# Kernel optimization log

Measured on AMD Instinct MI355X. Metric: run time of the kernel, lower is better.

## Reference

```python
import jax, jax.numpy as jnp
import numpy as np
import math

D_MODEL = 768
B, S = 8, 2048


def setup_inputs() -> dict:
    key = jax.random.key(0)
    k1, k2, k3, k4, k5 = jax.random.split(key, 5)
    return {
        "input": jax.random.normal(k1, (B, S, D_MODEL), dtype=jnp.float32),
        "attention_mask": jax.random.randint(k2, (B,), 0, S + 1, dtype=jnp.int32),
        "Wq": jax.random.normal(k3, (D_MODEL, D_MODEL), dtype=jnp.float32),
        "Wk": jax.random.normal(k4, (D_MODEL, D_MODEL), dtype=jnp.float32),
        "Wv": jax.random.normal(k5, (D_MODEL, D_MODEL), dtype=jnp.float32),
    }


def reference(input, attention_mask, Wq, Wk, Wv):
    d_model = Wq.shape[0]
    # QKV projections (v is computed in the original but never used in the output)
    q = jnp.matmul(input, Wq)  # [B,S,D]
    k = jnp.matmul(input, Wk)  # [B,S,D]
    v = jnp.matmul(input, Wv)  # [B,S,D] (dead in original forward output)
    # Per-sample QK^T, vectorized instead of the original python loop+cat
    attention_score = jnp.einsum("bqd,bkd->bqk", q, k) / math.sqrt(float(d_model) ** 3)
    # Ragged mask: positions (j,k) with j<len_i and k<len_i keep the score, else -1000.
    # Built with vectorized arange comparisons instead of the original triple python loop.
    idx = jnp.arange(attention_score.shape[1])  # [S]
    valid = idx[None, :] < attention_mask[:, None]  # [B,S]
    keep = valid[:, :, None] & valid[:, None, :]  # [B,S,S]
    mask_attention_score = jnp.where(keep, attention_score, jnp.float32(-1000.0))
    attention_score_n = jax.nn.softmax(mask_attention_score, axis=-1)  # computed but unused, as in original
    # Original returns UNMASKED, pre-softmax scores matmul'd with the raw input (not v).
    self_attention = jnp.einsum("bqk,bkd->bqd", attention_score, input)
    return self_attention
```

## Files before the change

### kernel.cpp

```cpp
#include <hip/hip_runtime.h>
#include <cmath>


typedef __attribute__((ext_vector_type(8))) short short8;
typedef __attribute__((ext_vector_type(4))) float f32x4;

__device__ __forceinline__ unsigned short f2bf(float f) {
    union { float f; unsigned int u; } v; v.f = f;
    unsigned int u = v.u;
    return (unsigned short)((u + 0x7FFFu + ((u >> 16) & 1u)) >> 16);
}

template <int NIT>
__device__ __forceinline__ void setup_stage(const unsigned short* base, int ld, int tid,
                                            const unsigned short* (&gp)[NIT])
{
    #pragma unroll
    for (int it = 0; it < NIT; ++it) {
        int slot = it * 256 + tid, r = slot >> 3, c = slot & 7;
        gp[it] = base + (size_t)r * ld + ((c ^ (r & 7)) << 3);
    }
}

template <int NIT>
__device__ __forceinline__ void stage_adv(const unsigned short* const (&gp)[NIT], int koff,
                                          unsigned short* ldsbase, int tid)
{
    #pragma unroll
    for (int it = 0; it < NIT; ++it) {
        unsigned short* lp = ldsbase + (size_t)(it * 256 + (tid & 192)) * 8;
        __builtin_amdgcn_global_load_lds(
            (__attribute__((address_space(1))) void*)(void*)(gp[it] + koff),
            (__attribute__((address_space(3))) void*)lp, 16, 0, 0);
    }
}

template <int F>
__device__ __forceinline__ void frag_offs(int wbase, int l15, int quad, int (&o)[F][2])
{
    #pragma unroll
    for (int i = 0; i < F; ++i) {
        int r = wbase + i * 16 + l15;
        o[i][0] = r * 64 + ((quad ^ (r & 7)) << 3);
        o[i][1] = r * 64 + (((quad + 4) ^ (r & 7)) << 3);
    }
}

template <int FM, int FN>
__device__ __forceinline__ void mfma_frags(const unsigned short* __restrict__ Al,
                                           const unsigned short* __restrict__ Bl,
                                           const int (&oA)[FM][2], const int (&oB)[FN][2],
                                           f32x4 (&acc)[FM][FN])
{
    short8 af[FM][2], bfr[FN][2];
    #pragma unroll
    for (int i = 0; i < FM; ++i) {
        af[i][0] = *reinterpret_cast<const short8*>(&Al[oA[i][0]]);
        af[i][1] = *reinterpret_cast<const short8*>(&Al[oA[i][1]]);
    }
    #pragma unroll
    for (int i = 0; i < FN; ++i) {
        bfr[i][0] = *reinterpret_cast<const short8*>(&Bl[oB[i][0]]);
        bfr[i][1] = *reinterpret_cast<const short8*>(&Bl[oB[i][1]]);
    }
    #pragma unroll
    for (int ks = 0; ks < 2; ++ks)
        #pragma unroll
        for (int mi = 0; mi < FM; ++mi)
            #pragma unroll
            for (int ni = 0; ni < FN; ++ni)
                acc[mi][ni] = __builtin_amdgcn_mfma_f32_16x16x32_bf16(
                    af[mi][ks], bfr[ni][ks], acc[mi][ni], 0, 0, 0);
}

template <int ROWS>
__device__ __forceinline__ void stage_f32(const float* __restrict__ src, unsigned short* lds,
                                          int ld, int tid)
{
    #pragma unroll
    for (int it = 0; it < ROWS / 32; ++it) {
        int slot = it * 256 + tid;
        int r = slot >> 3, c = slot & 7;
        const float* gp = src + (size_t)r * ld + c * 8;
        float4 a = *reinterpret_cast<const float4*>(gp);
        float4 d = *reinterpret_cast<const float4*>(gp + 4);
        union { short8 s; unsigned short u[8]; } v;
        v.u[0] = f2bf(a.x); v.u[1] = f2bf(a.y); v.u[2] = f2bf(a.z); v.u[3] = f2bf(a.w);
        v.u[4] = f2bf(d.x); v.u[5] = f2bf(d.y); v.u[6] = f2bf(d.z); v.u[7] = f2bf(d.w);
        *reinterpret_cast<short8*>(&lds[r * 64 + ((c ^ (r & 7)) << 3)]) = v.s;
    }
}

__device__ __forceinline__ void store_c(float* C, size_t i, float v) { C[i] = v; }
__device__ __forceinline__ void store_c(unsigned short* C, size_t i, float v) { C[i] = f2bf(v); }

template <int TM, int TN, typename CT>
__device__ __forceinline__ void epilogue(CT* __restrict__ C, f32x4 (&acc)[TM / 32][TN / 32],
                                         int rowBase, int colBase, int ldc, float alpha,
                                         int wr, int wc, int l15, int quad)
{
    #pragma unroll
    for (int mi = 0; mi < TM / 32; ++mi)
        #pragma unroll
        for (int ni = 0; ni < TN / 32; ++ni) {
            int col = colBase + wc + ni * 16 + l15;
            #pragma unroll
            for (int r = 0; r < 4; ++r) {
                int row = rowBase + wr + mi * 16 + quad * 4 + r;
                store_c(C, (size_t)row * ldc + col, alpha * acc[mi][ni][r]);
            }
        }
}

__global__ __launch_bounds__(256)
void prep(const float* __restrict__ X, unsigned short* __restrict__ Xt,
          unsigned short* __restrict__ Xbf)
{
    __shared__ unsigned short T[64 * 64];
    const int blk = blockIdx.x;
    const int b = blk & 7;
    const int tile = blk >> 3;
    const int s0 = (tile & 31) * 64;
    const int d0 = (tile >> 5) * 64;
    const float* Xb = X + (size_t)b * 2048 * 768;
    unsigned short* Xtb = Xt + (size_t)b * 2048 * 768;
    unsigned short* Xbb = Xbf + (size_t)b * 2048 * 768;

    const int mr = threadIdx.x >> 4;
    const int mc = threadIdx.x & 15;

    const float* src = &Xb[(size_t)(s0 + 4 * mr) * 768 + d0 + 4 * mc];
    float4 v0 = *reinterpret_cast<const float4*>(src);
    float4 v1 = *reinterpret_cast<const float4*>(src + 768);
    float4 v2 = *reinterpret_cast<const float4*>(src + 2 * 768);
    float4 v3 = *reinterpret_cast<const float4*>(src + 3 * 768);
    ushort4 r0 = { f2bf(v0.x), f2bf(v0.y), f2bf(v0.z), f2bf(v0.w) };
    ushort4 r1 = { f2bf(v1.x), f2bf(v1.y), f2bf(v1.z), f2bf(v1.w) };
    ushort4 r2 = { f2bf(v2.x), f2bf(v2.y), f2bf(v2.z), f2bf(v2.w) };
    ushort4 r3 = { f2bf(v3.x), f2bf(v3.y), f2bf(v3.z), f2bf(v3.w) };
    unsigned short* dstb = &Xbb[(size_t)(s0 + 4 * mr) * 768 + d0 + 4 * mc];
    *reinterpret_cast<ushort4*>(dstb)            = r0;
    *reinterpret_cast<ushort4*>(dstb + 768)      = r1;
    *reinterpret_cast<ushort4*>(dstb + 2 * 768)  = r2;
    *reinterpret_cast<ushort4*>(dstb + 3 * 768)  = r3;

    ushort4 c0 = { r0.x, r1.x, r2.x, r3.x };
    ushort4 c1 = { r0.y, r1.y, r2.y, r3.y };
    ushort4 c2 = { r0.z, r1.z, r2.z, r3.z };
    ushort4 c3 = { r0.w, r1.w, r2.w, r3.w };
    {
        int d;
        d = 4 * mc + 0; *reinterpret_cast<ushort4*>(&T[d * 64 + ((mr ^ (2 * (d & 7))) & 15) * 4]) = c0;
        d = 4 * mc + 1; *reinterpret_cast<ushort4*>(&T[d * 64 + ((mr ^ (2 * (d & 7))) & 15) * 4]) = c1;
        d = 4 * mc + 2; *reinterpret_cast<ushort4*>(&T[d * 64 + ((mr ^ (2 * (d & 7))) & 15) * 4]) = c2;
        d = 4 * mc + 3; *reinterpret_cast<ushort4*>(&T[d * 64 + ((mr ^ (2 * (d & 7))) & 15) * 4]) = c3;
    }
    __syncthreads();
    #pragma unroll
    for (int p = 0; p < 2; ++p) {
        int d  = p * 32 + (threadIdx.x >> 3);
        int q0 = 2 * (threadIdx.x & 7);
        int c  = (q0 ^ (2 * (d & 7))) & 15;
        short8 o = *reinterpret_cast<const short8*>(&T[d * 64 + c * 4]);
        *reinterpret_cast<short8*>(&Xtb[(size_t)(d0 + d) * 2048 + s0 + q0 * 4]) = o;
    }
}

__global__ __launch_bounds__(256)
void gemm_GP(const unsigned short* __restrict__ Xt, unsigned short* __restrict__ G16,
             const float* __restrict__ Wq, const float* __restrict__ Wk,
             unsigned short* __restrict__ P16)
{
    __shared__ unsigned short lds[2][(64 + 64) * 64];
    const int blk = blockIdx.x;
    const int tid = threadIdx.x, lane = tid & 63, wave = tid >> 6;
    const int l15 = lane & 15, quad = lane >> 4;
    const int wr = (wave >> 1) * 32, wc = (wave & 1) * 32;

    if (blk < 624) {
        const int b = blk & 7;
        const int u = blk >> 3;
        int ty = 0, rem = u, len = 12;
        while (rem >= len) { rem -= len; --len; ++ty; }
        const int tz = ty + rem;
        const bool diag = (ty == tz);

        const unsigned short* Xtb = Xt + (size_t)b * 768 * 2048;
        const unsigned short* A0 = Xtb + (size_t)ty * 64 * 2048;
        const unsigned short* B0 = Xtb + (size_t)tz * 64 * 2048;
        unsigned short* C = G16 + (size_t)b * 768 * 768;

        const unsigned short* gA[2]; const unsigned short* gB[2];
        setup_stage<2>(A0, 2048, tid, gA);
        setup_stage<2>(B0, 2048, tid, gB);
        int oA[2][2], oB[2][2];
        frag_offs<2>(wr, l15, quad, oA);
        frag_offs<2>(wc, l15, quad, oB);
        const int bbase = diag ? 0 : 64 * 64;

        f32x4 acc[2][2] = {};
        stage_adv<2>(gA, 0, &lds[0][0], tid);
        if (!diag) stage_adv<2>(gB, 0, &lds[0][64 * 64], tid);
        __syncthreads();

        const int nt = 32;
        for (int t = 0; t < nt; ++t) {
            const int cur = t & 1;
            if (t + 1 < nt) {
                stage_adv<2>(gA, (t + 1) * 64, &lds[cur ^ 1][0], tid);
                if (!diag) stage_adv<2>(gB, (t + 1) * 64, &lds[cur ^ 1][64 * 64], tid);
            }
            mfma_frags<2, 2>(&lds[cur][0], &lds[cur][bbase], oA, oB, acc);
            __syncthreads();
        }

        #pragma unroll
        for (int mi = 0; mi < 2; ++mi)
            #pragma unroll
            for (int ni = 0; ni < 2; ++ni) {
                int col = tz * 64 + wc + ni * 16 + l15;
                int row0 = ty * 64 + wr + mi * 16 + quad * 4;
                ushort4 m;
                m.x = f2bf(acc[mi][ni][0]);
                m.y = f2bf(acc[mi][ni][1]);
                m.z = f2bf(acc[mi][ni][2]);
                m.w = f2bf(acc[mi][ni][3]);
                C[(size_t)(row0 + 0) * 768 + col] = m.x;
                C[(size_t)(row0 + 1) * 768 + col] = m.y;
                C[(size_t)(row0 + 2) * 768 + col] = m.z;
                C[(size_t)(row0 + 3) * 768 + col] = m.w;
                if (!diag)
                    *reinterpret_cast<ushort4*>(&C[(size_t)col * 768 + row0]) = m;
            }
    } else {
        const int pb = blk - 624;
        const int ty = pb / 12, tz = pb - ty * 12;
        int oA[2][2], oB[2][2];
        frag_offs<2>(wr, l15, quad, oA);
        frag_offs<2>(wc, l15, quad, oB);
        f32x4 acc[2][2] = {};
        for (int k0 = 0; k0 < 768; k0 += 64) {
            stage_f32<64>(Wq + (size_t)ty * 64 * 768 + k0, &lds[0][0], 768, tid);
            stage_f32<64>(Wk + (size_t)tz * 64 * 768 + k0, &lds[0][64 * 64], 768, tid);
            __syncthreads();
            mfma_frags<2, 2>(&lds[0][0], &lds[0][64 * 64], oA, oB, acc);
            __syncthreads();
        }
        epilogue<64, 64, unsigned short>(P16, acc, ty * 64, tz * 64, 768, 1.0f,
                                         wr, wc, l15, quad);
    }
}

__global__ __launch_bounds__(256)
void gemm_Ht(const unsigned short* __restrict__ G16, const unsigned short* __restrict__ P16,
             unsigned short* __restrict__ Ht, float alpha)
{
    __shared__ unsigned short lds[2][(96 + 96) * 64];
    const int b = blockIdx.x, ty = blockIdx.y, tz = blockIdx.z;
    const int tid = threadIdx.x, lane = tid & 63, wave = tid >> 6;
    const int wr = (wave >> 1) * 48, wc = (wave & 1) * 48;
    const int l15 = lane & 15, quad = lane >> 4;

    const unsigned short* A0 = G16 + (size_t)b * 768 * 768 + (size_t)ty * 96 * 768;
    const unsigned short* B0 = P16 + (size_t)tz * 96 * 768;

    const unsigned short* gA[3]; const unsigned short* gB[3];
    setup_stage<3>(A0, 768, tid, gA);
    setup_stage<3>(B0, 768, tid, gB);
    int oA[3][2], oB[3][2];
    frag_offs<3>(wr, l15, quad, oA);
    frag_offs<3>(wc, l15, quad, oB);

    f32x4 acc[3][3] = {};
    stage_adv<3>(gA, 0, &lds[0][0], tid);
    stage_adv<3>(gB, 0, &lds[0][96 * 64], tid);
    __syncthreads();

    const int nt = 12;
    for (int t = 0; t < nt; ++t) {
        const int cur = t & 1;
        if (t + 1 < nt) {
            stage_adv<3>(gA, (t + 1) * 64, &lds[cur ^ 1][0], tid);
            stage_adv<3>(gB, (t + 1) * 64, &lds[cur ^ 1][96 * 64], tid);
        }
        mfma_frags<3, 3>(&lds[cur][0], &lds[cur][96 * 64], oA, oB, acc);
        __syncthreads();
    }
    epilogue<96, 96, unsigned short>(Ht + (size_t)b * 768 * 768, acc,
                                     ty * 96, tz * 96, 768, alpha, wr, wc, l15, quad);
}

__global__ __launch_bounds__(256)
void gemm_out(const unsigned short* __restrict__ Xbf, const unsigned short* __restrict__ Ht,
              float* __restrict__ out)
{
    __shared__ unsigned short lds[2][(128 + 128) * 64];
    const int b = blockIdx.x, ty = blockIdx.y, tz = blockIdx.z;
    const int tid = threadIdx.x, lane = tid & 63, wave = tid >> 6;
    const int wr = (wave >> 1) * 64, wc = (wave & 1) * 64;
    const int l15 = lane & 15, quad = lane >> 4;

    const unsigned short* A0 = Xbf + (size_t)b * 2048 * 768 + (size_t)ty * 128 * 768;
    const unsigned short* B0 = Ht + (size_t)b * 768 * 768 + (size_t)tz * 128 * 768;

    const unsigned short* gA[4]; const unsigned short* gB[4];
    setup_stage<4>(A0, 768, tid, gA);
    setup_stage<4>(B0, 768, tid, gB);
    int oA[4][2], oB[4][2];
    frag_offs<4>(wr, l15, quad, oA);
    frag_offs<4>(wc, l15, quad, oB);

    f32x4 acc[4][4] = {};
    stage_adv<4>(gA, 0, &lds[0][0], tid);
    stage_adv<4>(gB, 0, &lds[0][128 * 64], tid);
    __syncthreads();

    const int nt = 12;
    for (int t = 0; t < nt; ++t) {
        const int cur = t & 1;
        if (t + 1 < nt) {
            stage_adv<4>(gA, (t + 1) * 64, &lds[cur ^ 1][0], tid);
            stage_adv<4>(gB, (t + 1) * 64, &lds[cur ^ 1][128 * 64], tid);
        }
        mfma_frags<4, 4>(&lds[cur][0], &lds[cur][128 * 64], oA, oB, acc);
        __syncthreads();
    }
    epilogue<128, 128, float>(out + (size_t)b * 2048 * 768, acc,
                              ty * 128, tz * 128, 768, 1.0f, wr, wc, l15, quad);
}

extern "C" void kernel_launch(void* const* d_in, const int* in_sizes, int n_in,
                              void* d_out, int out_size, void* d_ws, size_t ws_size,
                              hipStream_t stream)
{
    const float* X  = (const float*)d_in[0];
    const float* Wq = (const float*)d_in[2];
    const float* Wk = (const float*)d_in[3];
    float* out = (float*)d_out;

    const int Bn = 8, S = 2048, D = 768;
    const float alpha = 1.0f / (768.0f * sqrtf(768.0f));
    const size_t szX  = (size_t)Bn * S * D;
    const size_t szDD = (size_t)Bn * D * D;

    unsigned short* Xt  = (unsigned short*)d_ws;
    unsigned short* Xbf = Xt + szX;
    unsigned short* P16 = Xbf + szX;
    unsigned short* G16 = P16 + (size_t)D * D;
    unsigned short* Ht  = G16 + szDD;

    prep<<<dim3(Bn * (S / 64) * (D / 64)), 256, 0, stream>>>(X, Xt, Xbf);

    gemm_GP<<<dim3(768), 256, 0, stream>>>(Xt, G16, Wq, Wk, P16);

    gemm_Ht<<<dim3(Bn, 8, 8), 256, 0, stream>>>(G16, P16, Ht, alpha);

    gemm_out<<<dim3(Bn, S / 128, 6), 256, 0, stream>>>(Xbf, Ht, out);
}
```

Before: 180.6 us.

## Fuse Ht and output GEMMs into one persistent kernel with per-batch grid barrier

```diff
diff --git a/kernel.cpp b/kernel.cpp
--- a/kernel.cpp
+++ b/kernel.cpp
@@ -9,6 +9,27 @@
     union { float f; unsigned int u; } v; v.f = f;
     unsigned int u = v.u;
     return (unsigned short)((u + 0x7FFFu + ((u >> 16) & 1u)) >> 16);
+}
+
+__device__ unsigned g_tbar[8][64];
+
+__device__ __forceinline__ void abarrier(unsigned* cnt, unsigned* gen, unsigned n)
+{
+    __syncthreads();
+    if (threadIdx.x == 0) {
+        __threadfence();
+        unsigned g = __hip_atomic_load(gen, __ATOMIC_RELAXED, __HIP_MEMORY_SCOPE_AGENT);
+        unsigned c = __hip_atomic_fetch_add(cnt, 1u, __ATOMIC_ACQ_REL, __HIP_MEMORY_SCOPE_AGENT);
+        if (c == n - 1u) {
+            __hip_atomic_store(cnt, 0u, __ATOMIC_RELAXED, __HIP_MEMORY_SCOPE_AGENT);
+            __hip_atomic_store(gen, g + 1u, __ATOMIC_RELEASE, __HIP_MEMORY_SCOPE_AGENT);
+        } else {
+            while (__hip_atomic_load(gen, __ATOMIC_RELAXED, __HIP_MEMORY_SCOPE_AGENT) == g)
+                __builtin_amdgcn_s_sleep(2);
+        }
+        __threadfence();
+    }
+    __syncthreads();
 }
 
 template <int NIT>
@@ -252,81 +273,74 @@
 }
 
 __global__ __launch_bounds__(256)
-void gemm_Ht(const unsigned short* __restrict__ G16, const unsigned short* __restrict__ P16,
-             unsigned short* __restrict__ Ht, float alpha)
-{
-    __shared__ unsigned short lds[2][(96 + 96) * 64];
-    const int b = blockIdx.x, ty = blockIdx.y, tz = blockIdx.z;
+void ht_out(const unsigned short* __restrict__ G16, const unsigned short* __restrict__ P16,
+            unsigned short* __restrict__ Ht, const unsigned short* __restrict__ Xbf,
+            float* __restrict__ out, float alpha)
+{
+    __shared__ unsigned short lds[(128 + 64) * 64];
+    const int blk = blockIdx.x;
+    const int b  = blk & 7;
+    const int lr = blk >> 3;
     const int tid = threadIdx.x, lane = tid & 63, wave = tid >> 6;
-    const int wr = (wave >> 1) * 48, wc = (wave & 1) * 48;
     const int l15 = lane & 15, quad = lane >> 4;
 
-    const unsigned short* A0 = G16 + (size_t)b * 768 * 768 + (size_t)ty * 96 * 768;
-    const unsigned short* B0 = P16 + (size_t)tz * 96 * 768;
-
-    const unsigned short* gA[3]; const unsigned short* gB[3];
-    setup_stage<3>(A0, 768, tid, gA);
-    setup_stage<3>(B0, 768, tid, gB);
-    int oA[3][2], oB[3][2];
-    frag_offs<3>(wr, l15, quad, oA);
-    frag_offs<3>(wc, l15, quad, oB);
-
-    f32x4 acc[3][3] = {};
-    stage_adv<3>(gA, 0, &lds[0][0], tid);
-    stage_adv<3>(gB, 0, &lds[0][96 * 64], tid);
-    __syncthreads();
-
-    const int nt = 12;
-    for (int t = 0; t < nt; ++t) {
-        const int cur = t & 1;
-        if (t + 1 < nt) {
-            stage_adv<3>(gA, (t + 1) * 64, &lds[cur ^ 1][0], tid);
-            stage_adv<3>(gB, (t + 1) * 64, &lds[cur ^ 1][96 * 64], tid);
-        }
-        mfma_frags<3, 3>(&lds[cur][0], &lds[cur][96 * 64], oA, oB, acc);
-        __syncthreads();
-    }
-    epilogue<96, 96, unsigned short>(Ht + (size_t)b * 768 * 768, acc,
-                                     ty * 96, tz * 96, 768, alpha, wr, wc, l15, quad);
-}
-
-__global__ __launch_bounds__(256)
-void gemm_out(const unsigned short* __restrict__ Xbf, const unsigned short* __restrict__ Ht,
-              float* __restrict__ out)
-{
-    __shared__ unsigned short lds[2][(128 + 128) * 64];
-    const int b = blockIdx.x, ty = blockIdx.y, tz = blockIdx.z;
-    const int tid = threadIdx.x, lane = tid & 63, wave = tid >> 6;
-    const int wr = (wave >> 1) * 64, wc = (wave & 1) * 64;
-    const int l15 = lane & 15, quad = lane >> 4;
-
-    const unsigned short* A0 = Xbf + (size_t)b * 2048 * 768 + (size_t)ty * 128 * 768;
-    const unsigned short* B0 = Ht + (size_t)b * 768 * 768 + (size_t)tz * 128 * 768;
-
-    const unsigned short* gA[4]; const unsigned short* gB[4];
-    setup_stage<4>(A0, 768, tid, gA);
-    setup_stage<4>(B0, 768, tid, gB);
-    int oA[4][2], oB[4][2];
-    frag_offs<4>(wr, l15, quad, oA);
-    frag_offs<4>(wc, l15, quad, oB);
-
-    f32x4 acc[4][4] = {};
-    stage_adv<4>(gA, 0, &lds[0][0], tid);
-    stage_adv<4>(gB, 0, &lds[0][128 * 64], tid);
-    __syncthreads();
-
-    const int nt = 12;
-    for (int t = 0; t < nt; ++t) {
-        const int cur = t & 1;
-        if (t + 1 < nt) {
-            stage_adv<4>(gA, (t + 1) * 64, &lds[cur ^ 1][0], tid);
-            stage_adv<4>(gB, (t + 1) * 64, &lds[cur ^ 1][128 * 64], tid);
-        }
-        mfma_frags<4, 4>(&lds[cur][0], &lds[cur][128 * 64], oA, oB, acc);
-        __syncthreads();
-    }
-    epilogue<128, 128, float>(out + (size_t)b * 2048 * 768, acc,
-                              ty * 128, tz * 128, 768, 1.0f, wr, wc, l15, quad);
+    {
+        const int wr = (wave >> 1) * 32, wc = (wave & 1) * 32;
+        int oA[2][2], oB[2][2];
+        frag_offs<2>(wr, l15, quad, oA);
+        frag_offs<2>(wc, l15, quad, oB);
+        const int nrep = (lr < 48) ? 2 : 1;
+        for (int rep = 0; rep < nrep; ++rep) {
+            const int u = lr + rep * 96;
+            const int ty = u / 12, tz = u - (u / 12) * 12;
+            const unsigned short* A0 = G16 + (size_t)b * 768 * 768 + (size_t)ty * 64 * 768;
+            const unsigned short* B0 = P16 + (size_t)tz * 64 * 768;
+            const unsigned short* gA[2]; const unsigned short* gB[2];
+            setup_stage<2>(A0, 768, tid, gA);
+            setup_stage<2>(B0, 768, tid, gB);
+            f32x4 acc[2][2] = {};
+            for (int k0 = 0; k0 < 768; k0 += 64) {
+                stage_adv<2>(gA, k0, lds, tid);
+                stage_adv<2>(gB, k0, lds + 64 * 64, tid);
+                __syncthreads();
+                mfma_frags<2, 2>(lds, lds + 64 * 64, oA, oB, acc);
+                __syncthreads();
+            }
+            epilogue<64, 64, unsigned short>(Ht + (size_t)b * 768 * 768, acc,
+                                             ty * 64, tz * 64, 768, alpha,
+                                             wr, wc, l15, quad);
+        }
+    }
+
+    abarrier(&g_tbar[b][0], &g_tbar[b][16], 96);
+
+    {
+        const int wr = (wave >> 1) * 64, wc = (wave & 1) * 32;
+        int oA[4][2], oB[2][2];
+        frag_offs<4>(wr, l15, quad, oA);
+        frag_offs<2>(wc, l15, quad, oB);
+        #pragma unroll
+        for (int rep = 0; rep < 2; ++rep) {
+            const int u = lr + rep * 96;
+            const int ty = u / 12, tz = u - (u / 12) * 12;
+            const unsigned short* A0 = Xbf + (size_t)b * 2048 * 768 + (size_t)ty * 128 * 768;
+            const unsigned short* B0 = Ht + (size_t)b * 768 * 768 + (size_t)tz * 64 * 768;
+            const unsigned short* gA[4]; const unsigned short* gB[2];
+            setup_stage<4>(A0, 768, tid, gA);
+            setup_stage<2>(B0, 768, tid, gB);
+            f32x4 acc[4][2] = {};
+            for (int k0 = 0; k0 < 768; k0 += 64) {
+                stage_adv<4>(gA, k0, lds, tid);
+                stage_adv<2>(gB, k0, lds + 128 * 64, tid);
+                __syncthreads();
+                mfma_frags<4, 2>(lds, lds + 128 * 64, oA, oB, acc);
+                __syncthreads();
+            }
+            epilogue<128, 64, float>(out + (size_t)b * 2048 * 768, acc,
+                                     ty * 128, tz * 64, 768, 1.0f,
+                                     wr, wc, l15, quad);
+        }
+    }
 }
 
 extern "C" void kernel_launch(void* const* d_in, const int* in_sizes, int n_in,
@@ -353,7 +367,5 @@
 
     gemm_GP<<<dim3(768), 256, 0, stream>>>(Xt, G16, Wq, Wk, P16);
 
-    gemm_Ht<<<dim3(Bn, 8, 8), 256, 0, stream>>>(G16, P16, Ht, alpha);
-
-    gemm_out<<<dim3(Bn, S / 128, 6), 256, 0, stream>>>(Xbf, Ht, out);
-}
+    ht_out<<<dim3(768), 256, 0, stream>>>(G16, P16, Ht, Xbf, out, alpha);
+}
```

After: 251.3 us. +39.1%, slower.
